# Kernel optimization log

Measured on AMD Instinct MI355X. Metric: run time of the kernel, lower is better.

## Reference

```python
import jax, jax.numpy as jnp
import numpy as np

S = 4096
F = 512  # in_features, head_num == 1 so per-head dim == F


def setup_inputs() -> dict:
    key = jax.random.key(0)
    ks = jax.random.split(key, 11)
    std = 0.02
    inp = {
        "q": jax.random.normal(ks[0], (1, S, F), jnp.float32),
        "k": jax.random.normal(ks[1], (1, S, F), jnp.float32),
        "v": jax.random.normal(ks[2], (1, S, F), jnp.float32),
        "Wq": jax.random.normal(ks[3], (F, F), jnp.float32) * std,
        "bq": jax.random.normal(ks[4], (F,), jnp.float32) * std,
        "Wk": jax.random.normal(ks[5], (F, F), jnp.float32) * std,
        "bk": jax.random.normal(ks[6], (F,), jnp.float32) * std,
        "Wv": jax.random.normal(ks[7], (F, F), jnp.float32) * std,
        "bv": jax.random.normal(ks[8], (F,), jnp.float32) * std,
        "Wo": jax.random.normal(ks[9], (F, F), jnp.float32) * std,
        "bo": jax.random.normal(ks[10], (F,), jnp.float32) * std,
    }
    return inp


def reference(q, k, v, Wq, bq, Wk, bk, Wv, bv, Wo, bo):
    dk = Wq.shape[0]  # head_num == 1 -> per-head dim equals in_features
    # q_k, q_v: projections of q WITHOUT activation (as in original forward)
    q_k = q @ Wk.T + bk            # (1, S, F)
    q_v = q @ Wv.T + bv            # (1, S, F)
    # activated projections (F.relu)
    qq = jax.nn.relu(q @ Wq.T + bq)[0]  # (S, F)
    kk = jax.nn.relu(k @ Wk.T + bk)[0]  # (S, F)
    vv = jax.nn.relu(v @ Wv.T + bv)[0]  # (S, F)
    # diagonal of qq @ q_k^T, computed without materializing the SxS matrix
    q_att = jnp.sum(qq * q_k[0], axis=-1, keepdims=True)  # (S, 1)
    scores = jnp.einsum('sd,td->st', qq, kk)               # (S, S)
    scores = jnp.concatenate([scores, q_att], axis=-1)     # (S, S+1)
    scores = scores / np.sqrt(dk + 1).astype(np.float32)
    attn = jax.nn.softmax(scores, axis=-1)                 # (S, S+1)
    res = attn[:, :-1] @ vv                                # (S, F)
    res = q_v[0] * q_att + res                             # elementwise fusion
    y = res[None]                                          # (1, S, F)
    y = jax.nn.relu(y @ Wo.T + bo)
    return y
```

## Files before the change

### kernel.cpp

```cpp
#include <hip/hip_runtime.h>
#include <math.h>

#define S_LEN 4096
#define F_DIM 512
#define PSPLIT 8
#define FIXED_M 4.0f
#define SCALE_QK 0.04415108f

typedef __attribute__((ext_vector_type(8))) short bf16x8;
typedef __attribute__((ext_vector_type(4))) float f32x4;

__device__ __forceinline__ unsigned short f2bf(float x) {
    union { float f; unsigned u; } v; v.f = x;
    unsigned r = v.u + 0x7fffu + ((v.u >> 16) & 1u);
    return (unsigned short)(r >> 16);
}
__device__ __forceinline__ float bf2f(unsigned short b) {
    union { unsigned u; float f; } v; v.u = ((unsigned)b) << 16;
    return v.f;
}
__device__ __forceinline__ void load_lds16(const void* g, void* l) {
    __builtin_amdgcn_global_load_lds(
        (const __attribute__((address_space(1))) unsigned int*)g,
        (__attribute__((address_space(3))) unsigned int*)l, 16, 0, 0);
}

struct CastArgs {
    const float* src[7];
    unsigned short* dst[7];
    int n4[7];
};
__global__ void cast_all(CastArgs a) {
    int r = blockIdx.y;
    int i = blockIdx.x * blockDim.x + threadIdx.x;
    if (i >= a.n4[r]) return;
    float4 v = ((const float4*)a.src[r])[i];
    ushort4 o;
    o.x = f2bf(v.x); o.y = f2bf(v.y); o.z = f2bf(v.z); o.w = f2bf(v.w);
    ((ushort4*)a.dst[r])[i] = o;
}

__global__ void transpose_bf16(const unsigned short* __restrict__ src,
                               unsigned short* __restrict__ dst) {
    __shared__ __align__(16) unsigned short tile[64][72];
    const int s0 = blockIdx.x * 64, f0 = blockIdx.y * 64;
    const int tid = threadIdx.x;
#pragma unroll
    for (int it = 0; it < 2; ++it) {
        int u = it * 256 + tid;
        int r = u >> 3, c = (u & 7) * 8;
        *(uint4*)&tile[r][c] = *(const uint4*)(src + (size_t)(s0 + r) * F_DIM + f0 + c);
    }
    __syncthreads();
#pragma unroll
    for (int it = 0; it < 2; ++it) {
        int u = it * 256 + tid;
        int fl = u >> 3, sc = (u & 7) * 8;
        unsigned short tmp[8];
#pragma unroll
        for (int i = 0; i < 8; ++i) tmp[i] = tile[sc + i][fl];
        *(uint4*)(dst + (size_t)(f0 + fl) * S_LEN + s0 + sc) = *(uint4*)tmp;
    }
}

struct GemmDesc {
    const unsigned short* X;
    const unsigned short* W;
    const float* bias;
    unsigned short* out_bf;
    float* out_f32;
    int relu;
};
struct GemmArgs { GemmDesc d[5]; };

#define FRAGA(qm) { _Pragma("unroll") for (int mt = 0; mt < 4; ++mt) { \
    const int ro = (aw + (qm) * 64 + mt * 16) * 64 + rbase; \
    af[mt][0] = *(const bf16x8*)&Ac[ro + q0]; \
    af[mt][1] = *(const bf16x8*)&Ac[ro + q1]; } }

#define FRAGB(qn) { _Pragma("unroll") for (int nt = 0; nt < 2; ++nt) { \
    const int ro = (bw + (qn) * 32 + nt * 16) * 64 + rbase; \
    bf[nt][0] = *(const bf16x8*)&Bc[ro + q0]; \
    bf[nt][1] = *(const bf16x8*)&Bc[ro + q1]; } }

#define MMQ(qm, qn) { __builtin_amdgcn_s_setprio(1); \
    _Pragma("unroll") for (int kh = 0; kh < 2; ++kh) \
    _Pragma("unroll") for (int mt = 0; mt < 4; ++mt) \
    _Pragma("unroll") for (int nt = 0; nt < 2; ++nt) \
      acc[(qm) * 4 + mt][(qn) * 2 + nt] = __builtin_amdgcn_mfma_f32_16x16x32_bf16( \
          af[mt][kh], bf[nt][kh], acc[(qm) * 4 + mt][(qn) * 2 + nt], 0, 0, 0); \
    __builtin_amdgcn_s_setprio(0); }

__device__ __forceinline__ void kloop256(const unsigned short* __restrict__ A, int lda,
                                         const unsigned short* __restrict__ B, int ldb,
                                         int m0, int n0, int kbase,
                                         unsigned short* smem, f32x4 acc[8][4]) {
    const int tid = threadIdx.x;
    const int w = tid >> 6, l = tid & 63;
    const int ln = l & 15, quad = l >> 4, lnx = l & 7;
    const int wm = w >> 2, wn = w & 3;
    const int srow = l >> 3;
    const int scol = (lnx ^ srow) * 8;
    const int rbase = ln * 64;
    const int q0 = (quad ^ lnx) * 8;
    const int q1 = ((4 + quad) ^ lnx) * 8;
    unsigned short* As = smem;
    unsigned short* Bs = smem + 32768;
    const unsigned short* Asrc = A + (size_t)(m0 + srow) * lda + kbase + scol;
    const unsigned short* Bsrc = B + (size_t)(n0 + srow) * ldb + kbase + scol;

    auto stageA = [&](int dd, int ktn) {
#pragma unroll
        for (int j = 0; j < 4; ++j) {
            int chunk = w * 4 + j;
            load_lds16(Asrc + (size_t)(chunk * 8) * lda + ktn * 64,
                       &As[dd * 16384 + chunk * 512]);
        }
    };
    auto stageB = [&](int dd, int ktn) {
#pragma unroll
        for (int j = 0; j < 4; ++j) {
            int chunk = w * 4 + j;
            load_lds16(Bsrc + (size_t)(chunk * 8) * ldb + ktn * 64,
                       &Bs[dd * 16384 + chunk * 512]);
        }
    };

    stageA(0, 0); stageB(0, 0);
    asm volatile("s_waitcnt vmcnt(0)" ::: "memory");
    __builtin_amdgcn_s_barrier();

#pragma unroll
    for (int kt = 0; kt < 8; ++kt) {
        const int d = kt & 1;
        const unsigned short* Ac = &As[d * 16384];
        const unsigned short* Bc = &Bs[d * 16384];
        const int aw = wm * 128, bw = wn * 64;
        bf16x8 af[4][2], bf[2][2];

        FRAGA(0); FRAGB(0);
        if (kt < 7) stageA(d ^ 1, kt + 1);
        __builtin_amdgcn_s_barrier();
        MMQ(0, 0);
        __builtin_amdgcn_s_barrier();

        FRAGB(1);
        if (kt < 7) stageB(d ^ 1, kt + 1);
        __builtin_amdgcn_s_barrier();
        MMQ(0, 1);
        __builtin_amdgcn_s_barrier();

        FRAGA(1);
        __builtin_amdgcn_s_barrier();
        MMQ(1, 1);
        __builtin_amdgcn_s_barrier();

        FRAGB(0);
        __builtin_amdgcn_s_barrier();
        MMQ(1, 0);
        asm volatile("s_waitcnt vmcnt(0)" ::: "memory");
        __builtin_amdgcn_s_barrier();
    }
}

__launch_bounds__(512, 2)
__global__ void gemm_proj2(GemmArgs args) {
    extern __shared__ unsigned short smem[];
    const GemmDesc d = args.d[blockIdx.y >> 1];
    const int n0 = (blockIdx.y & 1) * 256;
    const int m0 = blockIdx.x * 256;
    f32x4 acc[8][4];
    f32x4 z = {0.f, 0.f, 0.f, 0.f};
#pragma unroll
    for (int i = 0; i < 8; ++i)
#pragma unroll
        for (int j = 0; j < 4; ++j) acc[i][j] = z;

    kloop256(d.X, F_DIM, d.W, F_DIM, m0, n0, 0, smem, acc);

    const int tid = threadIdx.x;
    const int w = tid >> 6, l = tid & 63, quad = l >> 4, ln = l & 15;
    const int wm = w >> 2, wn = w & 3;
#pragma unroll
    for (int mi = 0; mi < 8; ++mi)
#pragma unroll
        for (int ni = 0; ni < 4; ++ni)
#pragma unroll
            for (int r = 0; r < 4; ++r) {
                int row = m0 + wm * 128 + mi * 16 + quad * 4 + r;
                int col = n0 + wn * 64 + ni * 16 + ln;
                float vv = acc[mi][ni][r] + d.bias[col];
                if (d.relu) vv = fmaxf(vv, 0.f);
                if (d.out_bf)  d.out_bf[(size_t)row * F_DIM + col] = f2bf(vv);
                if (d.out_f32) d.out_f32[(size_t)row * F_DIM + col] = vv;
            }
}

__launch_bounds__(512, 2)
__global__ void gemm_exp2(const unsigned short* __restrict__ X,
                          const unsigned short* __restrict__ W,
                          unsigned short* __restrict__ P,
                          float* __restrict__ lpart) {
    extern __shared__ unsigned short smem[];
    const int m0 = blockIdx.x * 256, n0 = blockIdx.y * 256;
    f32x4 acc[8][4];
    f32x4 z = {0.f, 0.f, 0.f, 0.f};
#pragma unroll
    for (int i = 0; i < 8; ++i)
#pragma unroll
        for (int j = 0; j < 4; ++j) acc[i][j] = z;

    kloop256(X, F_DIM, W, F_DIM, m0, n0, 0, smem, acc);

    const int tid = threadIdx.x;
    const int w = tid >> 6, l = tid & 63, quad = l >> 4, ln = l & 15;
    const int wm = w >> 2, wn = w & 3;
#pragma unroll
    for (int mi = 0; mi < 8; ++mi)
#pragma unroll
        for (int r = 0; r < 4; ++r) {
            int row = m0 + wm * 128 + mi * 16 + quad * 4 + r;
            float rs = 0.f;
#pragma unroll
            for (int ni = 0; ni < 4; ++ni) {
                int col = n0 + wn * 64 + ni * 16 + ln;
                float p = __expf(acc[mi][ni][r] * SCALE_QK - FIXED_M);
                P[(size_t)row * S_LEN + col] = f2bf(p);
                rs += p;
            }
            rs += __shfl_xor(rs, 1);
            rs += __shfl_xor(rs, 2);
            rs += __shfl_xor(rs, 4);
            rs += __shfl_xor(rs, 8);
            if (ln == 0) lpart[(size_t)row * 64 + blockIdx.y * 4 + wn] = rs;
        }
}

__launch_bounds__(512, 2)
__global__ void gemm_pv2(const unsigned short* __restrict__ P,
                         const unsigned short* __restrict__ vt,
                         unsigned short* __restrict__ O_p) {
    extern __shared__ unsigned short smem[];
    const int nb = blockIdx.y & 1, split = blockIdx.y >> 1;
    const int m0 = blockIdx.x * 256, n0 = nb * 256;
    f32x4 acc[8][4];
    f32x4 z = {0.f, 0.f, 0.f, 0.f};
#pragma unroll
    for (int i = 0; i < 8; ++i)
#pragma unroll
        for (int j = 0; j < 4; ++j) acc[i][j] = z;

    kloop256(P, S_LEN, vt, S_LEN, m0, n0, split * (S_LEN / PSPLIT), smem, acc);

    unsigned short* Op = O_p + (size_t)split * S_LEN * F_DIM;
    const int tid = threadIdx.x;
    const int w = tid >> 6, l = tid & 63, quad = l >> 4, ln = l & 15;
    const int wm = w >> 2, wn = w & 3;
#pragma unroll
    for (int mi = 0; mi < 8; ++mi)
#pragma unroll
        for (int ni = 0; ni < 4; ++ni)
#pragma unroll
            for (int r = 0; r < 4; ++r) {
                int row = m0 + wm * 128 + mi * 16 + quad * 4 + r;
                int col = n0 + wn * 64 + ni * 16 + ln;
                Op[(size_t)row * F_DIM + col] = f2bf(acc[mi][ni][r]);
            }
}

#define GEMM_KLOOP(XPTR, LDX, WPTR, LDW, KBEG, KEND)                                  \
    for (int k0 = (KBEG); k0 < (KEND); k0 += 64) {                                    \
        __syncthreads();                                                              \
        _Pragma("unroll")                                                             \
        for (int i = 0; i < 2; ++i) {                                                 \
            int c = w * 2 + i;                                                        \
            _Pragma("unroll")                                                         \
            for (int kh = 0; kh < 2; ++kh) {                                          \
                load_lds16((XPTR) + (size_t)(m0 + c * 16 + ln) * (LDX) + k0 + kh * 32 + quad * 8, \
                           &As[(c * 2 + kh) * 512]);                                  \
                load_lds16((WPTR) + (size_t)(n0 + c * 16 + ln) * (LDW) + k0 + kh * 32 + quad * 8, \
                           &Bs[(c * 2 + kh) * 512]);                                  \
            }                                                                         \
        }                                                                             \
        __syncthreads();                                                              \
        _Pragma("unroll")                                                             \
        for (int kh = 0; kh < 2; ++kh) {                                              \
            bf16x8 af2[4], bfr2[4];                                                   \
            _Pragma("unroll")                                                         \
            for (int mt = 0; mt < 4; ++mt)                                            \
                af2[mt] = *(const bf16x8*)&As[((wr * 4 + mt) * 2 + kh) * 512 + l * 8]; \
            _Pragma("unroll")                                                         \
            for (int nt = 0; nt < 4; ++nt)                                            \
                bfr2[nt] = *(const bf16x8*)&Bs[((wc * 4 + nt) * 2 + kh) * 512 + l * 8]; \
            _Pragma("unroll")                                                         \
            for (int mt = 0; mt < 4; ++mt)                                            \
                _Pragma("unroll")                                                     \
                for (int nt = 0; nt < 4; ++nt)                                        \
                    acc[mt][nt] = __builtin_amdgcn_mfma_f32_16x16x32_bf16(            \
                        af2[mt], bfr2[nt], acc[mt][nt], 0, 0, 0);                     \
        }                                                                             \
    }

__launch_bounds__(256, 2)
__global__ void gemm_final(const unsigned short* __restrict__ X,
                           const unsigned short* __restrict__ W,
                           const float* __restrict__ bias,
                           float* __restrict__ out) {
    __shared__ __align__(16) unsigned short As[16 * 512];
    __shared__ __align__(16) unsigned short Bs[16 * 512];
    const int n0 = blockIdx.y * 128;
    const int m0 = blockIdx.x * 128;
    const int tid = threadIdx.x;
    const int w = tid >> 6, l = tid & 63, quad = l >> 4, ln = l & 15;
    const int wr = w >> 1, wc = w & 1;

    f32x4 acc[4][4];
    f32x4 zero4 = {0.f, 0.f, 0.f, 0.f};
#pragma unroll
    for (int i = 0; i < 4; ++i)
#pragma unroll
        for (int j = 0; j < 4; ++j) acc[i][j] = zero4;

    GEMM_KLOOP(X, F_DIM, W, F_DIM, 0, F_DIM)

#pragma unroll
    for (int mt = 0; mt < 4; ++mt)
#pragma unroll
        for (int nt = 0; nt < 4; ++nt)
#pragma unroll
            for (int r = 0; r < 4; ++r) {
                int row = m0 + wr * 64 + mt * 16 + quad * 4 + r;
                int col = n0 + wc * 64 + nt * 16 + ln;
                out[(size_t)row * F_DIM + col] =
                    fmaxf(acc[mt][nt][r] + bias[col], 0.f);
            }
}

__global__ void combine_kernel(const unsigned short* __restrict__ O_p,
                               const float* __restrict__ lpart,
                               const unsigned short* __restrict__ qq,
                               const unsigned short* __restrict__ qk,
                               const unsigned short* __restrict__ qv,
                               unsigned short* __restrict__ res_bf) {
    int row = blockIdx.x;
    int t = threadIdx.x;
    int wv = t >> 6, l = t & 63;
    __shared__ float ws[4];

    ushort4 a = *(const ushort4*)(qq + (size_t)row * F_DIM + t * 4);
    ushort4 b = *(const ushort4*)(qk + (size_t)row * F_DIM + t * 4);
    float dotp = bf2f(a.x) * bf2f(b.x) + bf2f(a.y) * bf2f(b.y) +
                 bf2f(a.z) * bf2f(b.z) + bf2f(a.w) * bf2f(b.w);
    float lp = (t < 64) ? lpart[(size_t)row * 64 + t] : 0.f;
#pragma unroll
    for (int off = 32; off >= 1; off >>= 1) {
        dotp += __shfl_xor(dotp, off);
        lp += __shfl_xor(lp, off);
    }
    if (l == 0) { ws[wv] = dotp; ws[2 + wv] = lp; }
    __syncthreads();
    float qa = ws[0] + ws[1];
    float denom = __expf(qa * SCALE_QK - FIXED_M) + ws[2] + ws[3];
    float inv = 1.f / denom;

    float4 s = {0.f, 0.f, 0.f, 0.f};
#pragma unroll
    for (int i = 0; i < PSPLIT; ++i) {
        ushort4 o = *(const ushort4*)(O_p + ((size_t)i * S_LEN + row) * F_DIM + t * 4);
        s.x += bf2f(o.x); s.y += bf2f(o.y); s.z += bf2f(o.z); s.w += bf2f(o.w);
    }
    ushort4 qvv = *(const ushort4*)(qv + (size_t)row * F_DIM + t * 4);
    ushort4 o;
    o.x = f2bf(bf2f(qvv.x) * qa + s.x * inv);
    o.y = f2bf(bf2f(qvv.y) * qa + s.y * inv);
    o.z = f2bf(bf2f(qvv.z) * qa + s.z * inv);
    o.w = f2bf(bf2f(qvv.w) * qa + s.w * inv);
    *(ushort4*)(res_bf + (size_t)row * F_DIM + t * 4) = o;
}

extern "C" void kernel_launch(void* const* d_in, const int* in_sizes, int n_in,
                              void* d_out, int out_size, void* d_ws, size_t ws_size,
                              hipStream_t stream) {
    const float* q  = (const float*)d_in[0];
    const float* k  = (const float*)d_in[1];
    const float* v  = (const float*)d_in[2];
    const float* Wq = (const float*)d_in[3];
    const float* bq = (const float*)d_in[4];
    const float* Wk = (const float*)d_in[5];
    const float* bk = (const float*)d_in[6];
    const float* Wv = (const float*)d_in[7];
    const float* bv = (const float*)d_in[8];
    const float* Wo = (const float*)d_in[9];
    const float* bo = (const float*)d_in[10];
    float* out = (float*)d_out;

    char* p = (char*)d_ws;
    auto alloc = [&](size_t bytes) -> char* {
        char* r = p; p += (bytes + 255) & ~(size_t)255; return r;
    };
    const size_t SF = (size_t)S_LEN * F_DIM;
    unsigned short* q_bf  = (unsigned short*)alloc(SF * 2);
    unsigned short* k_bf  = (unsigned short*)alloc(SF * 2);
    unsigned short* v_bf  = (unsigned short*)alloc(SF * 2);
    unsigned short* qq_bf = (unsigned short*)alloc(SF * 2);
    unsigned short* kk_bf = (unsigned short*)alloc(SF * 2);
    unsigned short* vv_bf = (unsigned short*)alloc(SF * 2);
    unsigned short* vt_bf = (unsigned short*)alloc(SF * 2);
    unsigned short* qk_bf = (unsigned short*)alloc(SF * 2);
    unsigned short* qv_bf = (unsigned short*)alloc(SF * 2);
    unsigned short* res_bf = (unsigned short*)alloc(SF * 2);
    unsigned short* wq_bf = (unsigned short*)alloc((size_t)F_DIM * F_DIM * 2);
    unsigned short* wk_bf = (unsigned short*)alloc((size_t)F_DIM * F_DIM * 2);
    unsigned short* wv_bf = (unsigned short*)alloc((size_t)F_DIM * F_DIM * 2);
    unsigned short* wo_bf = (unsigned short*)alloc((size_t)F_DIM * F_DIM * 2);
    unsigned short* P_bf  = (unsigned short*)alloc((size_t)S_LEN * S_LEN * 2);
    float* lpart = (float*)alloc((size_t)S_LEN * 64 * 4);
    unsigned short* O_p = (unsigned short*)alloc((size_t)PSPLIT * SF * 2);

    static int attr_done = 0;
    if (!attr_done) {
        hipFuncSetAttribute((const void*)gemm_proj2,
                            hipFuncAttributeMaxDynamicSharedMemorySize, 131072);
        hipFuncSetAttribute((const void*)gemm_exp2,
                            hipFuncAttributeMaxDynamicSharedMemorySize, 131072);
        hipFuncSetAttribute((const void*)gemm_pv2,
                            hipFuncAttributeMaxDynamicSharedMemorySize, 131072);
        attr_done = 1;
    }

    CastArgs ca;
    ca.src[0] = q;  ca.dst[0] = q_bf;  ca.n4[0] = (int)(SF / 4);
    ca.src[1] = k;  ca.dst[1] = k_bf;  ca.n4[1] = (int)(SF / 4);
    ca.src[2] = v;  ca.dst[2] = v_bf;  ca.n4[2] = (int)(SF / 4);
    ca.src[3] = Wq; ca.dst[3] = wq_bf; ca.n4[3] = F_DIM * F_DIM / 4;
    ca.src[4] = Wk; ca.dst[4] = wk_bf; ca.n4[4] = F_DIM * F_DIM / 4;
    ca.src[5] = Wv; ca.dst[5] = wv_bf; ca.n4[5] = F_DIM * F_DIM / 4;
    ca.src[6] = Wo; ca.dst[6] = wo_bf; ca.n4[6] = F_DIM * F_DIM / 4;
    cast_all<<<dim3((unsigned)(SF / 4 / 256), 7), 256, 0, stream>>>(ca);

    GemmArgs ga;
    ga.d[0] = { q_bf, wq_bf, bq, qq_bf, nullptr, 1 };
    ga.d[1] = { k_bf, wk_bf, bk, kk_bf, nullptr, 1 };
    ga.d[2] = { v_bf, wv_bf, bv, vv_bf, nullptr, 1 };
    ga.d[3] = { q_bf, wk_bf, bk, qk_bf, nullptr, 0 };
    ga.d[4] = { q_bf, wv_bf, bv, qv_bf, nullptr, 0 };
    gemm_proj2<<<dim3(S_LEN / 256, 10), 512, 131072, stream>>>(ga);

    transpose_bf16<<<dim3(S_LEN / 64, F_DIM / 64), 256, 0, stream>>>(vv_bf, vt_bf);

    gemm_exp2<<<dim3(S_LEN / 256, S_LEN / 256), 512, 131072, stream>>>(qq_bf, kk_bf, P_bf, lpart);

    gemm_pv2<<<dim3(S_LEN / 256, 2 * PSPLIT), 512, 131072, stream>>>(P_bf, vt_bf, O_p);

    combine_kernel<<<S_LEN, 128, 0, stream>>>(O_p, lpart, qq_bf, qk_bf, qv_bf, res_bf);

    gemm_final<<<dim3(S_LEN / 128, 4), 256, 0, stream>>>(res_bf, wo_bf, bo, out);
}
```

Baseline: 200.8 us.

## Shrink GEMM tiles to 256x128 with a triple-buffered LDS pipeline

The shared GEMM main loop now computes 256x128 output tiles instead of 256x256, and keeps three LDS stages, prefetching two K-tiles ahead. A partial vmcnt wait replaces the previous full drain each iteration. The projection, QK^T-exp and PV kernels move to flat 1D grids with twice as many blocks, and the lpart indexing is remapped to match. The aim is better load hiding and finer work distribution across CUs, at the cost of lower data reuse per tile, more LDS per block (147 KB) and more blocks than CUs.

After: 209.1 us. 4.2% more time.

```diff
diff --git a/kernel.cpp b/kernel.cpp
--- a/kernel.cpp
+++ b/kernel.cpp
@@ -4,6 +4,7 @@
 #define S_LEN 4096
 #define F_DIM 512
 #define PSPLIT 8
+#define NTILES 8
 #define FIXED_M 4.0f
 #define SCALE_QK 0.04415108f
 
@@ -73,123 +74,135 @@
 };
 struct GemmArgs { GemmDesc d[5]; };
 
-#define FRAGA(qm) { _Pragma("unroll") for (int mt = 0; mt < 4; ++mt) { \
-    const int ro = (aw + (qm) * 64 + mt * 16) * 64 + rbase; \
-    af[mt][0] = *(const bf16x8*)&Ac[ro + q0]; \
-    af[mt][1] = *(const bf16x8*)&Ac[ro + q1]; } }
-
-#define FRAGB(qn) { _Pragma("unroll") for (int nt = 0; nt < 2; ++nt) { \
-    const int ro = (bw + (qn) * 32 + nt * 16) * 64 + rbase; \
-    bf[nt][0] = *(const bf16x8*)&Bc[ro + q0]; \
-    bf[nt][1] = *(const bf16x8*)&Bc[ro + q1]; } }
-
-#define MMQ(qm, qn) { __builtin_amdgcn_s_setprio(1); \
-    _Pragma("unroll") for (int kh = 0; kh < 2; ++kh) \
-    _Pragma("unroll") for (int mt = 0; mt < 4; ++mt) \
-    _Pragma("unroll") for (int nt = 0; nt < 2; ++nt) \
-      acc[(qm) * 4 + mt][(qn) * 2 + nt] = __builtin_amdgcn_mfma_f32_16x16x32_bf16( \
-          af[mt][kh], bf[nt][kh], acc[(qm) * 4 + mt][(qn) * 2 + nt], 0, 0, 0); \
-    __builtin_amdgcn_s_setprio(0); }
-
-__device__ __forceinline__ void kloop256(const unsigned short* __restrict__ A, int lda,
-                                         const unsigned short* __restrict__ B, int ldb,
-                                         int m0, int n0, int kbase,
-                                         unsigned short* smem, f32x4 acc[8][4]) {
+__device__ __forceinline__ void kloop256x128(
+        const unsigned short* __restrict__ A, int lda,
+        const unsigned short* __restrict__ B, int ldb,
+        int m0, int n0, int kbase,
+        unsigned short* smem, f32x4 acc[4][4]) {
     const int tid = threadIdx.x;
     const int w = tid >> 6, l = tid & 63;
     const int ln = l & 15, quad = l >> 4, lnx = l & 7;
-    const int wm = w >> 2, wn = w & 3;
+    const int wm = w >> 1, wn = w & 1;
     const int srow = l >> 3;
     const int scol = (lnx ^ srow) * 8;
-    const int rbase = ln * 64;
     const int q0 = (quad ^ lnx) * 8;
     const int q1 = ((4 + quad) ^ lnx) * 8;
     unsigned short* As = smem;
-    unsigned short* Bs = smem + 32768;
+    unsigned short* Bs = smem + 3 * 16384;
     const unsigned short* Asrc = A + (size_t)(m0 + srow) * lda + kbase + scol;
     const unsigned short* Bsrc = B + (size_t)(n0 + srow) * ldb + kbase + scol;
 
-    auto stageA = [&](int dd, int ktn) {
+    auto stage = [&](int bufi, int ktn) {
 #pragma unroll
         for (int j = 0; j < 4; ++j) {
             int chunk = w * 4 + j;
             load_lds16(Asrc + (size_t)(chunk * 8) * lda + ktn * 64,
-                       &As[dd * 16384 + chunk * 512]);
+                       &As[bufi * 16384 + chunk * 512]);
+        }
+#pragma unroll
+        for (int j = 0; j < 2; ++j) {
+            int chunk = w * 2 + j;
+            load_lds16(Bsrc + (size_t)(chunk * 8) * ldb + ktn * 64,
+                       &Bs[bufi * 8192 + chunk * 512]);
         }
     };
-    auto stageB = [&](int dd, int ktn) {
-#pragma unroll
-        for (int j = 0; j < 4; ++j) {
-            int chunk = w * 4 + j;
-            load_lds16(Bsrc + (size_t)(chunk * 8) * ldb + ktn * 64,
-                       &Bs[dd * 16384 + chunk * 512]);
-        }
-    };
-
-    stageA(0, 0); stageB(0, 0);
-    asm volatile("s_waitcnt vmcnt(0)" ::: "memory");
+
+    stage(0, 0);
+    stage(1, 1);
+    asm volatile("s_waitcnt vmcnt(6)" ::: "memory");
     __builtin_amdgcn_s_barrier();
 
 #pragma unroll
-    for (int kt = 0; kt < 8; ++kt) {
-        const int d = kt & 1;
-        const unsigned short* Ac = &As[d * 16384];
-        const unsigned short* Bc = &Bs[d * 16384];
-        const int aw = wm * 128, bw = wn * 64;
-        bf16x8 af[4][2], bf[2][2];
-
-        FRAGA(0); FRAGB(0);
-        if (kt < 7) stageA(d ^ 1, kt + 1);
+    for (int kt = 0; kt < NTILES; ++kt) {
+        const int b = kt % 3;
+        const unsigned short* Ac = &As[b * 16384];
+        const unsigned short* Bc = &Bs[b * 8192];
+        const int aw = wm * 64, bw = wn * 64;
+        bf16x8 af[2][2], bfr[4][2];
+
+#pragma unroll
+        for (int mi = 0; mi < 2; ++mi) {
+            int ro = (aw + mi * 16 + ln) * 64;
+            af[mi][0] = *(const bf16x8*)&Ac[ro + q0];
+            af[mi][1] = *(const bf16x8*)&Ac[ro + q1];
+        }
+#pragma unroll
+        for (int ni = 0; ni < 4; ++ni) {
+            int ro = (bw + ni * 16 + ln) * 64;
+            bfr[ni][0] = *(const bf16x8*)&Bc[ro + q0];
+            bfr[ni][1] = *(const bf16x8*)&Bc[ro + q1];
+        }
+        if (kt < NTILES - 2) stage((kt + 2) % 3, kt + 2);
         __builtin_amdgcn_s_barrier();
-        MMQ(0, 0);
+        __builtin_amdgcn_s_setprio(1);
+#pragma unroll
+        for (int kh = 0; kh < 2; ++kh)
+#pragma unroll
+            for (int mi = 0; mi < 2; ++mi)
+#pragma unroll
+                for (int ni = 0; ni < 4; ++ni)
+                    acc[mi][ni] = __builtin_amdgcn_mfma_f32_16x16x32_bf16(
+                        af[mi][kh], bfr[ni][kh], acc[mi][ni], 0, 0, 0);
+        __builtin_amdgcn_s_setprio(0);
         __builtin_amdgcn_s_barrier();
 
-        FRAGB(1);
-        if (kt < 7) stageB(d ^ 1, kt + 1);
+        bf16x8 ag[2][2];
+#pragma unroll
+        for (int mi = 0; mi < 2; ++mi) {
+            int ro = (aw + 32 + mi * 16 + ln) * 64;
+            ag[mi][0] = *(const bf16x8*)&Ac[ro + q0];
+            ag[mi][1] = *(const bf16x8*)&Ac[ro + q1];
+        }
         __builtin_amdgcn_s_barrier();
-        MMQ(0, 1);
+        __builtin_amdgcn_s_setprio(1);
+#pragma unroll
+        for (int kh = 0; kh < 2; ++kh)
+#pragma unroll
+            for (int mi = 0; mi < 2; ++mi)
+#pragma unroll
+                for (int ni = 0; ni < 4; ++ni)
+                    acc[2 + mi][ni] = __builtin_amdgcn_mfma_f32_16x16x32_bf16(
+                        ag[mi][kh], bfr[ni][kh], acc[2 + mi][ni], 0, 0, 0);
+        __builtin_amdgcn_s_setprio(0);
+        if (kt < NTILES - 2) {
+            asm volatile("s_waitcnt vmcnt(6)" ::: "memory");
+        } else if (kt == NTILES - 2) {
+            asm volatile("s_waitcnt vmcnt(0)" ::: "memory");
+        }
         __builtin_amdgcn_s_barrier();
-
-        FRAGA(1);
-        __builtin_amdgcn_s_barrier();
-        MMQ(1, 1);
-        __builtin_amdgcn_s_barrier();
-
-        FRAGB(0);
-        __builtin_amdgcn_s_barrier();
-        MMQ(1, 0);
-        asm volatile("s_waitcnt vmcnt(0)" ::: "memory");
-        __builtin_amdgcn_s_barrier();
-    }
-}
+    }
+}
+
 
 __launch_bounds__(512, 2)
 __global__ void gemm_proj2(GemmArgs args) {
     extern __shared__ unsigned short smem[];
-    const GemmDesc d = args.d[blockIdx.y >> 1];
-    const int n0 = (blockIdx.y & 1) * 256;
-    const int m0 = blockIdx.x * 256;
-    f32x4 acc[8][4];
+    const int bid = blockIdx.x;
+    const int g = bid >> 6, r2 = bid & 63;
+    const GemmDesc d = args.d[g];
+    const int m0 = (r2 & 15) * 256;
+    const int n0 = (r2 >> 4) * 128;
+    f32x4 acc[4][4];
     f32x4 z = {0.f, 0.f, 0.f, 0.f};
 #pragma unroll
-    for (int i = 0; i < 8; ++i)
+    for (int i = 0; i < 4; ++i)
 #pragma unroll
         for (int j = 0; j < 4; ++j) acc[i][j] = z;
 
-    kloop256(d.X, F_DIM, d.W, F_DIM, m0, n0, 0, smem, acc);
+    kloop256x128(d.X, F_DIM, d.W, F_DIM, m0, n0, 0, smem, acc);
 
     const int tid = threadIdx.x;
     const int w = tid >> 6, l = tid & 63, quad = l >> 4, ln = l & 15;
-    const int wm = w >> 2, wn = w & 3;
-#pragma unroll
-    for (int mi = 0; mi < 8; ++mi)
+    const int wm = w >> 1, wn = w & 1;
+#pragma unroll
+    for (int a = 0; a < 4; ++a)
 #pragma unroll
         for (int ni = 0; ni < 4; ++ni)
 #pragma unroll
             for (int r = 0; r < 4; ++r) {
-                int row = m0 + wm * 128 + mi * 16 + quad * 4 + r;
+                int row = m0 + wm * 64 + a * 16 + quad * 4 + r;
                 int col = n0 + wn * 64 + ni * 16 + ln;
-                float vv = acc[mi][ni][r] + d.bias[col];
+                float vv = acc[a][ni][r] + d.bias[col];
                 if (d.relu) vv = fmaxf(vv, 0.f);
                 if (d.out_bf)  d.out_bf[(size_t)row * F_DIM + col] = f2bf(vv);
                 if (d.out_f32) d.out_f32[(size_t)row * F_DIM + col] = vv;
@@ -202,29 +215,32 @@
                           unsigned short* __restrict__ P,
                           float* __restrict__ lpart) {
     extern __shared__ unsigned short smem[];
-    const int m0 = blockIdx.x * 256, n0 = blockIdx.y * 256;
-    f32x4 acc[8][4];
+    const int bid = blockIdx.x;
+    const int m0 = (bid & 15) * 256;
+    const int ntile = bid >> 4;
+    const int n0 = ntile * 128;
+    f32x4 acc[4][4];
     f32x4 z = {0.f, 0.f, 0.f, 0.f};
 #pragma unroll
-    for (int i = 0; i < 8; ++i)
+    for (int i = 0; i < 4; ++i)
 #pragma unroll
         for (int j = 0; j < 4; ++j) acc[i][j] = z;
 
-    kloop256(X, F_DIM, W, F_DIM, m0, n0, 0, smem, acc);
+    kloop256x128(X, F_DIM, W, F_DIM, m0, n0, 0, smem, acc);
 
     const int tid = threadIdx.x;
     const int w = tid >> 6, l = tid & 63, quad = l >> 4, ln = l & 15;
-    const int wm = w >> 2, wn = w & 3;
-#pragma unroll
-    for (int mi = 0; mi < 8; ++mi)
+    const int wm = w >> 1, wn = w & 1;
+#pragma unroll
+    for (int a = 0; a < 4; ++a)
 #pragma unroll
         for (int r = 0; r < 4; ++r) {
-            int row = m0 + wm * 128 + mi * 16 + quad * 4 + r;
+            int row = m0 + wm * 64 + a * 16 + quad * 4 + r;
             float rs = 0.f;
 #pragma unroll
             for (int ni = 0; ni < 4; ++ni) {
                 int col = n0 + wn * 64 + ni * 16 + ln;
-                float p = __expf(acc[mi][ni][r] * SCALE_QK - FIXED_M);
+                float p = __expf(acc[a][ni][r] * SCALE_QK - FIXED_M);
                 P[(size_t)row * S_LEN + col] = f2bf(p);
                 rs += p;
             }
@@ -232,7 +248,7 @@
             rs += __shfl_xor(rs, 2);
             rs += __shfl_xor(rs, 4);
             rs += __shfl_xor(rs, 8);
-            if (ln == 0) lpart[(size_t)row * 64 + blockIdx.y * 4 + wn] = rs;
+            if (ln == 0) lpart[(size_t)row * 64 + ntile * 2 + wn] = rs;
         }
 }
 
@@ -241,30 +257,33 @@
                          const unsigned short* __restrict__ vt,
                          unsigned short* __restrict__ O_p) {
     extern __shared__ unsigned short smem[];
-    const int nb = blockIdx.y & 1, split = blockIdx.y >> 1;
-    const int m0 = blockIdx.x * 256, n0 = nb * 256;
-    f32x4 acc[8][4];
+    const int bid = blockIdx.x;
+    const int m0 = (bid & 15) * 256;
+    const int y = bid >> 4;
+    const int n0 = (y & 3) * 128;
+    const int split = y >> 2;
+    f32x4 acc[4][4];
     f32x4 z = {0.f, 0.f, 0.f, 0.f};
 #pragma unroll
-    for (int i = 0; i < 8; ++i)
+    for (int i = 0; i < 4; ++i)
 #pragma unroll
         for (int j = 0; j < 4; ++j) acc[i][j] = z;
 
-    kloop256(P, S_LEN, vt, S_LEN, m0, n0, split * (S_LEN / PSPLIT), smem, acc);
+    kloop256x128(P, S_LEN, vt, S_LEN, m0, n0, split * (S_LEN / PSPLIT), smem, acc);
 
     unsigned short* Op = O_p + (size_t)split * S_LEN * F_DIM;
     const int tid = threadIdx.x;
     const int w = tid >> 6, l = tid & 63, quad = l >> 4, ln = l & 15;
-    const int wm = w >> 2, wn = w & 3;
-#pragma unroll
-    for (int mi = 0; mi < 8; ++mi)
+    const int wm = w >> 1, wn = w & 1;
+#pragma unroll
+    for (int a = 0; a < 4; ++a)
 #pragma unroll
         for (int ni = 0; ni < 4; ++ni)
 #pragma unroll
             for (int r = 0; r < 4; ++r) {
-                int row = m0 + wm * 128 + mi * 16 + quad * 4 + r;
+                int row = m0 + wm * 64 + a * 16 + quad * 4 + r;
                 int col = n0 + wn * 64 + ni * 16 + ln;
-                Op[(size_t)row * F_DIM + col] = f2bf(acc[mi][ni][r]);
+                Op[(size_t)row * F_DIM + col] = f2bf(acc[a][ni][r]);
             }
 }
 
@@ -420,11 +439,11 @@
     static int attr_done = 0;
     if (!attr_done) {
         hipFuncSetAttribute((const void*)gemm_proj2,
-                            hipFuncAttributeMaxDynamicSharedMemorySize, 131072);
+                            hipFuncAttributeMaxDynamicSharedMemorySize, 147456);
         hipFuncSetAttribute((const void*)gemm_exp2,
-                            hipFuncAttributeMaxDynamicSharedMemorySize, 131072);
+                            hipFuncAttributeMaxDynamicSharedMemorySize, 147456);
         hipFuncSetAttribute((const void*)gemm_pv2,
-                            hipFuncAttributeMaxDynamicSharedMemorySize, 131072);
+                            hipFuncAttributeMaxDynamicSharedMemorySize, 147456);
         attr_done = 1;
     }
 
@@ -444,13 +463,13 @@
     ga.d[2] = { v_bf, wv_bf, bv, vv_bf, nullptr, 1 };
     ga.d[3] = { q_bf, wk_bf, bk, qk_bf, nullptr, 0 };
     ga.d[4] = { q_bf, wv_bf, bv, qv_bf, nullptr, 0 };
-    gemm_proj2<<<dim3(S_LEN / 256, 10), 512, 131072, stream>>>(ga);
+    gemm_proj2<<<dim3(320), 512, 147456, stream>>>(ga);
 
     transpose_bf16<<<dim3(S_LEN / 64, F_DIM / 64), 256, 0, stream>>>(vv_bf, vt_bf);
 
-    gemm_exp2<<<dim3(S_LEN / 256, S_LEN / 256), 512, 131072, stream>>>(qq_bf, kk_bf, P_bf, lpart);
-
-    gemm_pv2<<<dim3(S_LEN / 256, 2 * PSPLIT), 512, 131072, stream>>>(P_bf, vt_bf, O_p);
+    gemm_exp2<<<dim3(512), 512, 147456, stream>>>(qq_bf, kk_bf, P_bf, lpart);
+
+    gemm_pv2<<<dim3(512), 512, 147456, stream>>>(P_bf, vt_bf, O_p);
 
     combine_kernel<<<S_LEN, 128, 0, stream>>>(O_p, lpart, qq_bf, qk_bf, qv_bf, res_bf);
 
```

## Fuse QK^T exp and PV GEMMs into a flash-style kernel keeping P in LDS

Applied to the files above, without the earlier changes.

Replaces the separate score/exp kernel, which wrote a full 4096x4096 bf16 P matrix to global memory, and the PV GEMM that read it back, with one fused kernel. Each block takes 128 query rows and a 512-key split, computes S tiles with double-buffered LDS staging, exponentiates them with the fixed max into swizzled LDS, and immediately multiplies by V^T tiles. This removes the large P round trip through HBM and one launch. In exchange the launch shrinks to 256 blocks with 128-row tiles, and Q tiles are re-staged for every KV chunk, so utilisation and reuse may be lower.

Result: slower. 254.2 us (+26.6%).

```diff
diff --git a/kernel.cpp b/kernel.cpp
--- a/kernel.cpp
+++ b/kernel.cpp
@@ -197,74 +197,170 @@
 }
 
 __launch_bounds__(512, 2)
-__global__ void gemm_exp2(const unsigned short* __restrict__ X,
-                          const unsigned short* __restrict__ W,
-                          unsigned short* __restrict__ P,
-                          float* __restrict__ lpart) {
+__global__ void gemm_fa(const unsigned short* __restrict__ qq,
+                        const unsigned short* __restrict__ kk,
+                        const unsigned short* __restrict__ vt,
+                        unsigned short* __restrict__ O_p,
+                        float* __restrict__ lpart) {
     extern __shared__ unsigned short smem[];
-    const int m0 = blockIdx.x * 256, n0 = blockIdx.y * 256;
-    f32x4 acc[8][4];
+    unsigned short* AsU = smem;
+    unsigned short* BsU = smem + 16384;
+    unsigned short* PsU = smem + 49152;
+    const int bid = blockIdx.x;
+    const int m0 = (bid & 31) * 128;
+    const int split = bid >> 5;
+
+    const int tid = threadIdx.x;
+    const int w = tid >> 6, l = tid & 63;
+    const int ln = l & 15, quad = l >> 4, lnx = l & 7;
+    const int wm = w >> 2, wn = w & 3;
+    const int srow = l >> 3;
+    const int scol = (lnx ^ srow) * 8;
+    const int q0 = (quad ^ lnx) * 8;
+    const int q1 = ((4 + quad) ^ lnx) * 8;
+
+    f32x4 o[4][8];
+    float rs[4][4];
     f32x4 z = {0.f, 0.f, 0.f, 0.f};
 #pragma unroll
-    for (int i = 0; i < 8; ++i)
-#pragma unroll
-        for (int j = 0; j < 4; ++j) acc[i][j] = z;
-
-    kloop256(X, F_DIM, W, F_DIM, m0, n0, 0, smem, acc);
-
-    const int tid = threadIdx.x;
-    const int w = tid >> 6, l = tid & 63, quad = l >> 4, ln = l & 15;
-    const int wm = w >> 2, wn = w & 3;
-#pragma unroll
-    for (int mi = 0; mi < 8; ++mi)
+    for (int i = 0; i < 4; ++i) {
+#pragma unroll
+        for (int jj = 0; jj < 8; ++jj) o[i][jj] = z;
+#pragma unroll
+        for (int jj = 0; jj < 4; ++jj) rs[i][jj] = 0.f;
+    }
+
+    const unsigned short* Aq = qq + (size_t)(m0 + srow) * F_DIM + scol;
+
+    for (int j = 0; j < 4; ++j) {
+        const int kvb = split * 512 + j * 128;
+        const unsigned short* Bk = kk + (size_t)(kvb + srow) * F_DIM + scol;
+
+        f32x4 sa[4][2];
+#pragma unroll
+        for (int i = 0; i < 4; ++i) { sa[i][0] = z; sa[i][1] = z; }
+
+        auto stageQ = [&](int dd, int kt) {
+#pragma unroll
+            for (int jj = 0; jj < 2; ++jj) {
+                int chunk = w * 2 + jj;
+                load_lds16(Aq + (size_t)(chunk * 8) * F_DIM + kt * 64,
+                           &AsU[dd * 8192 + chunk * 512]);
+                load_lds16(Bk + (size_t)(chunk * 8) * F_DIM + kt * 64,
+                           &BsU[dd * 8192 + chunk * 512]);
+            }
+        };
+        stageQ(0, 0);
+#pragma unroll
+        for (int kt = 0; kt < 8; ++kt) {
+            const int d = kt & 1;
+            asm volatile("s_waitcnt vmcnt(0)" ::: "memory");
+            __builtin_amdgcn_s_barrier();
+            bf16x8 af[4][2], bf[2][2];
+#pragma unroll
+            for (int mt = 0; mt < 4; ++mt) {
+                int ro = d * 8192 + (wm * 64 + mt * 16 + ln) * 64;
+                af[mt][0] = *(const bf16x8*)&AsU[ro + q0];
+                af[mt][1] = *(const bf16x8*)&AsU[ro + q1];
+            }
+#pragma unroll
+            for (int nt = 0; nt < 2; ++nt) {
+                int ro = d * 8192 + (wn * 32 + nt * 16 + ln) * 64;
+                bf[nt][0] = *(const bf16x8*)&BsU[ro + q0];
+                bf[nt][1] = *(const bf16x8*)&BsU[ro + q1];
+            }
+            if (kt < 7) stageQ(d ^ 1, kt + 1);
+            __builtin_amdgcn_s_setprio(1);
+#pragma unroll
+            for (int kh = 0; kh < 2; ++kh)
+#pragma unroll
+                for (int mt = 0; mt < 4; ++mt)
+#pragma unroll
+                    for (int nt = 0; nt < 2; ++nt)
+                        sa[mt][nt] = __builtin_amdgcn_mfma_f32_16x16x32_bf16(
+                            af[mt][kh], bf[nt][kh], sa[mt][nt], 0, 0, 0);
+            __builtin_amdgcn_s_setprio(0);
+        }
+        __builtin_amdgcn_s_barrier();
+
+#pragma unroll
+        for (int mt = 0; mt < 4; ++mt)
+#pragma unroll
+            for (int nt = 0; nt < 2; ++nt)
+#pragma unroll
+                for (int r = 0; r < 4; ++r) {
+                    int prow = wm * 64 + mt * 16 + quad * 4 + r;
+                    int pcol = wn * 32 + nt * 16 + ln;
+                    float p = __expf(sa[mt][nt][r] * SCALE_QK - FIXED_M);
+                    rs[mt][r] += p;
+                    int cb = pcol >> 3;
+                    PsU[prow * 128 + (((cb & 7) ^ (prow & 7)) | (cb & 8)) * 8 +
+                        (pcol & 7)] = f2bf(p);
+                }
+
+#pragma unroll
+        for (int kh2 = 0; kh2 < 2; ++kh2) {
+#pragma unroll
+            for (int jj = 0; jj < 8; ++jj) {
+                int chunk = w * 8 + jj;
+                load_lds16(vt + (size_t)(chunk * 8 + srow) * S_LEN + kvb +
+                               kh2 * 64 + scol,
+                           &smem[chunk * 512]);
+            }
+            __syncthreads();
+#pragma unroll
+            for (int kh = 0; kh < 2; ++kh) {
+                bf16x8 pa[4], pb[8];
+#pragma unroll
+                for (int mt = 0; mt < 4; ++mt) {
+                    int arow = wm * 64 + mt * 16 + ln;
+                    int cb = kh2 * 8 + kh * 4 + quad;
+                    pa[mt] = *(const bf16x8*)&PsU[arow * 128 +
+                        (((cb & 7) ^ (arow & 7)) | (cb & 8)) * 8];
+                }
+#pragma unroll
+                for (int nt = 0; nt < 8; ++nt) {
+                    int brow = wn * 128 + nt * 16 + ln;
+                    pb[nt] = *(const bf16x8*)&smem[brow * 64 + (kh ? q1 : q0)];
+                }
+                __builtin_amdgcn_s_setprio(1);
+#pragma unroll
+                for (int mt = 0; mt < 4; ++mt)
+#pragma unroll
+                    for (int nt = 0; nt < 8; ++nt)
+                        o[mt][nt] = __builtin_amdgcn_mfma_f32_16x16x32_bf16(
+                            pa[mt], pb[nt], o[mt][nt], 0, 0, 0);
+                __builtin_amdgcn_s_setprio(0);
+            }
+            __builtin_amdgcn_s_barrier();
+        }
+    }
+
+#pragma unroll
+    for (int mt = 0; mt < 4; ++mt)
 #pragma unroll
         for (int r = 0; r < 4; ++r) {
-            int row = m0 + wm * 128 + mi * 16 + quad * 4 + r;
-            float rs = 0.f;
-#pragma unroll
-            for (int ni = 0; ni < 4; ++ni) {
-                int col = n0 + wn * 64 + ni * 16 + ln;
-                float p = __expf(acc[mi][ni][r] * SCALE_QK - FIXED_M);
-                P[(size_t)row * S_LEN + col] = f2bf(p);
-                rs += p;
-            }
-            rs += __shfl_xor(rs, 1);
-            rs += __shfl_xor(rs, 2);
-            rs += __shfl_xor(rs, 4);
-            rs += __shfl_xor(rs, 8);
-            if (ln == 0) lpart[(size_t)row * 64 + blockIdx.y * 4 + wn] = rs;
+            float v = rs[mt][r];
+            v += __shfl_xor(v, 1);
+            v += __shfl_xor(v, 2);
+            v += __shfl_xor(v, 4);
+            v += __shfl_xor(v, 8);
+            if (ln == 0) {
+                int row = m0 + wm * 64 + mt * 16 + quad * 4 + r;
+                lpart[(size_t)row * 32 + split * 4 + wn] = v;
+            }
         }
-}
-
-__launch_bounds__(512, 2)
-__global__ void gemm_pv2(const unsigned short* __restrict__ P,
-                         const unsigned short* __restrict__ vt,
-                         unsigned short* __restrict__ O_p) {
-    extern __shared__ unsigned short smem[];
-    const int nb = blockIdx.y & 1, split = blockIdx.y >> 1;
-    const int m0 = blockIdx.x * 256, n0 = nb * 256;
-    f32x4 acc[8][4];
-    f32x4 z = {0.f, 0.f, 0.f, 0.f};
-#pragma unroll
-    for (int i = 0; i < 8; ++i)
-#pragma unroll
-        for (int j = 0; j < 4; ++j) acc[i][j] = z;
-
-    kloop256(P, S_LEN, vt, S_LEN, m0, n0, split * (S_LEN / PSPLIT), smem, acc);
 
     unsigned short* Op = O_p + (size_t)split * S_LEN * F_DIM;
-    const int tid = threadIdx.x;
-    const int w = tid >> 6, l = tid & 63, quad = l >> 4, ln = l & 15;
-    const int wm = w >> 2, wn = w & 3;
-#pragma unroll
-    for (int mi = 0; mi < 8; ++mi)
-#pragma unroll
-        for (int ni = 0; ni < 4; ++ni)
+#pragma unroll
+    for (int mt = 0; mt < 4; ++mt)
+#pragma unroll
+        for (int nt = 0; nt < 8; ++nt)
 #pragma unroll
             for (int r = 0; r < 4; ++r) {
-                int row = m0 + wm * 128 + mi * 16 + quad * 4 + r;
-                int col = n0 + wn * 64 + ni * 16 + ln;
-                Op[(size_t)row * F_DIM + col] = f2bf(acc[mi][ni][r]);
+                int row = m0 + wm * 64 + mt * 16 + quad * 4 + r;
+                int col = wn * 128 + nt * 16 + ln;
+                Op[(size_t)row * F_DIM + col] = f2bf(o[mt][nt][r]);
             }
 }
 
@@ -351,7 +447,7 @@
     ushort4 b = *(const ushort4*)(qk + (size_t)row * F_DIM + t * 4);
     float dotp = bf2f(a.x) * bf2f(b.x) + bf2f(a.y) * bf2f(b.y) +
                  bf2f(a.z) * bf2f(b.z) + bf2f(a.w) * bf2f(b.w);
-    float lp = (t < 64) ? lpart[(size_t)row * 64 + t] : 0.f;
+    float lp = (t < 32) ? lpart[(size_t)row * 32 + t] : 0.f;
 #pragma unroll
     for (int off = 32; off >= 1; off >>= 1) {
         dotp += __shfl_xor(dotp, off);
@@ -413,17 +509,14 @@
     unsigned short* wk_bf = (unsigned short*)alloc((size_t)F_DIM * F_DIM * 2);
     unsigned short* wv_bf = (unsigned short*)alloc((size_t)F_DIM * F_DIM * 2);
     unsigned short* wo_bf = (unsigned short*)alloc((size_t)F_DIM * F_DIM * 2);
-    unsigned short* P_bf  = (unsigned short*)alloc((size_t)S_LEN * S_LEN * 2);
-    float* lpart = (float*)alloc((size_t)S_LEN * 64 * 4);
+    float* lpart = (float*)alloc((size_t)S_LEN * 32 * 4);
     unsigned short* O_p = (unsigned short*)alloc((size_t)PSPLIT * SF * 2);
 
     static int attr_done = 0;
     if (!attr_done) {
         hipFuncSetAttribute((const void*)gemm_proj2,
                             hipFuncAttributeMaxDynamicSharedMemorySize, 131072);
-        hipFuncSetAttribute((const void*)gemm_exp2,
-                            hipFuncAttributeMaxDynamicSharedMemorySize, 131072);
-        hipFuncSetAttribute((const void*)gemm_pv2,
+        hipFuncSetAttribute((const void*)gemm_fa,
                             hipFuncAttributeMaxDynamicSharedMemorySize, 131072);
         attr_done = 1;
     }
@@ -448,9 +541,7 @@
 
     transpose_bf16<<<dim3(S_LEN / 64, F_DIM / 64), 256, 0, stream>>>(vv_bf, vt_bf);
 
-    gemm_exp2<<<dim3(S_LEN / 256, S_LEN / 256), 512, 131072, stream>>>(qq_bf, kk_bf, P_bf, lpart);
-
-    gemm_pv2<<<dim3(S_LEN / 256, 2 * PSPLIT), 512, 131072, stream>>>(P_bf, vt_bf, O_p);
+    gemm_fa<<<dim3(256), 512, 131072, stream>>>(qq_bf, kk_bf, vt_bf, O_p, lpart);
 
     combine_kernel<<<S_LEN, 128, 0, stream>>>(O_p, lpart, qq_bf, qk_bf, qv_bf, res_bf);
 
```
